# Kernel tuning notes

Measured on AMD Instinct MI355X. Metric: run time of the kernel, lower is better.

## Reference

```python
import jax, jax.numpy as jnp
import numpy as np

STRIDES = (8, 16, 32, 64)
IMG = 640
B, G, C = 32, 128, 80
REG_MAX = 7
CENTER_RADIUS = 2.5
TOPK = 10
IOU_W, CLS_W = 3.0, 1.0
VFL_ALPHA, VFL_GAMMA = 0.75, 2.0


def _make_priors():
    out = []
    for s in STRIDES:
        n = IMG // s
        ys = (np.arange(n, dtype=np.float32) + 0.5) * s
        xs = (np.arange(n, dtype=np.float32) + 0.5) * s
        yy, xx = np.meshgrid(ys, xs, indexing='ij')
        cx, cy = xx.ravel(), yy.ravel()
        ss = np.full_like(cx, float(s))
        out.append(np.stack([cx, cy, ss, ss], -1))
    return jnp.asarray(np.concatenate(out, 0), jnp.float32)  # (8500, 4)


def setup_inputs() -> dict:
    key = jax.random.key(0)
    k1, k2, k3, k4, k5, k6 = jax.random.split(key, 6)
    priors = _make_priors()
    N = priors.shape[0]
    # decoded xyxy boxes centered near each prior
    off = jax.random.normal(k1, (B, N, 2), dtype=jnp.float32) * 8.0
    wh = jax.random.uniform(k2, (B, N, 2), minval=8.0, maxval=160.0)
    ctr = priors[None, :, :2] + off
    decoded_bboxes = jnp.concatenate([ctr - wh * 0.5, ctr + wh * 0.5], -1)
    cls_pred = jax.random.uniform(k3, (B, N, C), minval=1e-4, maxval=1.0 - 1e-4)
    reg_pred = jax.random.normal(k4, (B, N, 4 * (REG_MAX + 1)), dtype=jnp.float32)
    gctr = jax.random.uniform(k5, (B, G, 2), minval=50.0, maxval=IMG - 50.0)
    gwh = jax.random.uniform(jax.random.fold_in(k5, 1), (B, G, 2), minval=20.0, maxval=300.0)
    gt_bboxes = jnp.concatenate([gctr - gwh * 0.5, gctr + gwh * 0.5], -1)
    gt_labels = jax.random.randint(k6, (B, G), 0, C)
    return {"priors": priors, "decoded_bboxes": decoded_bboxes, "cls_pred": cls_pred,
            "reg_pred": reg_pred, "gt_bboxes": gt_bboxes, "gt_labels": gt_labels}


def _pairwise_iou(a, b):
    # a: (N,4), b: (G,4) xyxy -> (N,G)
    area_a = (a[:, 2] - a[:, 0]) * (a[:, 3] - a[:, 1])
    area_b = (b[:, 2] - b[:, 0]) * (b[:, 3] - b[:, 1])
    tl = jnp.maximum(a[:, None, :2], b[None, :, :2])
    br = jnp.minimum(a[:, None, 2:], b[None, :, 2:])
    wh = jnp.clip(br - tl, 0.0)
    inter = wh[..., 0] * wh[..., 1]
    return inter / (area_a[:, None] + area_b[None, :] - inter + 1e-16)


def _giou_loss(pred, tgt):
    # aligned rows, xyxy; returns (N,)
    tl = jnp.maximum(pred[:, :2], tgt[:, :2])
    br = jnp.minimum(pred[:, 2:], tgt[:, 2:])
    wh = jnp.clip(br - tl, 0.0)
    inter = wh[:, 0] * wh[:, 1]
    ap = jnp.clip(pred[:, 2] - pred[:, 0], 0.0) * jnp.clip(pred[:, 3] - pred[:, 1], 0.0)
    at = jnp.clip(tgt[:, 2] - tgt[:, 0], 0.0) * jnp.clip(tgt[:, 3] - tgt[:, 1], 0.0)
    union = ap + at - inter
    iou = inter / (union + 1e-16)
    ctl = jnp.minimum(pred[:, :2], tgt[:, :2])
    cbr = jnp.maximum(pred[:, 2:], tgt[:, 2:])
    cwh = jnp.clip(cbr - ctl, 0.0)
    ac = cwh[:, 0] * cwh[:, 1]
    return 1.0 - (iou - (ac - union) / (ac + 1e-16))


def _simota(priors, dec, clsp, gtb, gtl):
    # single image. priors (N,4), dec (N,4), clsp (N,C), gtb (G,4), gtl (G,)
    nG = gtb.shape[0]
    cx, cy = priors[:, 0:1], priors[:, 1:2]
    sw, sh = priors[:, 2:3], priors[:, 3:4]
    # in-gt-box test: min of 4 edge distances > 0  -> (N,G)
    in_box = jnp.minimum(jnp.minimum(cx - gtb[None, :, 0], cy - gtb[None, :, 1]),
                         jnp.minimum(gtb[None, :, 2] - cx, gtb[None, :, 3] - cy)) > 0
    gcx = (gtb[:, 0] + gtb[:, 2]) * 0.5
    gcy = (gtb[:, 1] + gtb[:, 3]) * 0.5
    in_ctr = jnp.minimum(jnp.minimum(cx - (gcx[None] - CENTER_RADIUS * sw),
                                     cy - (gcy[None] - CENTER_RADIUS * sh)),
                         jnp.minimum(gcx[None] + CENTER_RADIUS * sw - cx,
                                     gcy[None] + CENTER_RADIUS * sh - cy)) > 0
    valid = in_box.any(1) | in_ctr.any(1)          # (N,)
    in_both = in_box & in_ctr                      # (N,G)
    ious = _pairwise_iou(dec, gtb)                 # (N,G)
    ious_m = jnp.where(valid[:, None], ious, 0.0)
    iou_cost = -jnp.log(ious + 1e-8)
    p = jnp.clip(clsp, 1e-7, 1.0 - 1e-7)
    neg = -jnp.log1p(-p)                           # (N,C)
    pos = -jnp.log(p)
    # sum_c BCE(p_nc, onehot_g) = sum_neg - neg[:,label_g] + pos[:,label_g]
    cls_cost = neg.sum(-1)[:, None] - neg[:, gtl] + pos[:, gtl]   # (N,G)
    cost = (CLS_W * cls_cost + IOU_W * iou_cost
            + 1e5 * (~in_both).astype(cost_dtype := clsp.dtype)
            + 1e8 * (~valid)[:, None].astype(cost_dtype))
    # dynamic-k per gt from sum of top-10 IoUs (invalid priors contribute 0)
    topk_ious = jax.lax.top_k(ious_m.T, TOPK)[0]                  # (G,TOPK)
    dyn_k = jnp.maximum(topk_ious.sum(-1).astype(jnp.int32), 1)   # (G,)
    # rank of each prior per gt (ascending cost); select dyn_k cheapest
    order = jnp.argsort(cost, axis=0)
    ranks = jnp.argsort(order, axis=0)
    matching = ranks < dyn_k[None, :]                             # (N,G) bool
    # resolve priors matched to >1 gt: keep lowest-cost gt
    multi = matching.sum(1) > 1
    best = jnp.argmin(cost, axis=1)
    matching = jnp.where(multi[:, None], jax.nn.one_hot(best, nG, dtype=bool), matching)
    fg = matching.any(1)
    mgt = jnp.argmax(matching, axis=1)
    mious = (matching * ious).sum(1)
    return fg, mgt, mious


def _image_loss(priors, dec, clsp, regp, gtb, gtl):
    sg = jax.lax.stop_gradient
    fg, mgt, mious = _simota(sg(priors), sg(dec), sg(clsp), sg(gtb), gtl)
    N = priors.shape[0]
    tscore = jnp.where(fg, mious, 0.0)             # (N,) soft target score
    lbl = gtl[mgt]                                 # (N,)
    # Varifocal loss (probabilities in, like the BCE-on-probs assigner)
    tgt = jax.nn.one_hot(lbl, C, dtype=clsp.dtype) * tscore[:, None]
    p = jnp.clip(clsp, 1e-7, 1.0 - 1e-7)
    bce = -(tgt * jnp.log(p) + (1.0 - tgt) * jnp.log1p(-p))
    w = jnp.where(tgt > 0, tgt, VFL_ALPHA * p ** VFL_GAMMA)
    vfl = (bce * w).sum()
    # GIoU on positives, weighted by target score
    ab = gtb[mgt]                                  # assigned gt box per prior (N,4)
    giou_sum = (_giou_loss(dec, ab) * tscore).sum()
    # DFL: distances from prior center to gt edges in stride units
    ctr, s = priors[:, :2], priors[:, 2:3]
    d = jnp.stack([ctr[:, 0] - ab[:, 0], ctr[:, 1] - ab[:, 1],
                   ab[:, 2] - ctr[:, 0], ab[:, 3] - ctr[:, 1]], -1) / s
    t = jnp.clip(d, 0.0, REG_MAX - 0.1)            # (N,4)
    logits = regp.reshape(N, 4, REG_MAX + 1)
    logp = jax.nn.log_softmax(logits, -1)
    tl_ = t.astype(jnp.int32)
    tr_ = jnp.minimum(tl_ + 1, REG_MAX)
    wl = (tl_ + 1).astype(t.dtype) - t
    wr = t - tl_.astype(t.dtype)
    ce = -(jnp.take_along_axis(logp, tl_[..., None], -1)[..., 0] * wl
           + jnp.take_along_axis(logp, tr_[..., None], -1)[..., 0] * wr)
    dfl_sum = (ce.sum(-1) * tscore).sum()
    return vfl, giou_sum, dfl_sum, fg.sum().astype(clsp.dtype), tscore.sum()


def _forward(priors, decoded_bboxes, cls_pred, reg_pred, gt_bboxes, gt_labels):
    vfl, gi, df, npos, nscore = jax.vmap(_image_loss, in_axes=(None, 0, 0, 0, 0, 0))(
        priors, decoded_bboxes, cls_pred, reg_pred, gt_bboxes, gt_labels)
    npos_t = jnp.maximum(npos.sum(), 1.0)
    ns_t = jnp.maximum(nscore.sum(), 1.0)
    return vfl.sum() / npos_t + 2.0 * gi.sum() / ns_t + 0.25 * df.sum() / ns_t


def reference(priors, decoded_bboxes, cls_pred, reg_pred, gt_bboxes, gt_labels):
    return _forward(priors, decoded_bboxes, cls_pred, reg_pred, gt_bboxes, gt_labels)
```

## Files before the change

kernel.cpp:

```cpp
#include <hip/hip_runtime.h>
#include <cstdint>
#include <cstddef>

#define NP    8500
#define BS    32
#define NGT   128
#define NCLS  80
#define TOPKK 10

typedef unsigned long long u64;
typedef unsigned int u32;

static __device__ __forceinline__ float iou_prec(const float4 a, const float4 b) {
  float area_a = (a.z - a.x) * (a.w - a.y);
  float area_b = (b.z - b.x) * (b.w - b.y);
  float tlx = fmaxf(a.x, b.x), tly = fmaxf(a.y, b.y);
  float brx = fminf(a.z, b.z), bry = fminf(a.w, b.w);
  float ww = fmaxf(brx - tlx, 0.f), hh = fmaxf(bry - tly, 0.f);
  float inter = ww * hh;
  return inter / (area_a + area_b - inter + 1e-16f);
}

static __device__ __forceinline__ float iou_fast(const float4 a, const float4 b) {
  float area_a = (a.z - a.x) * (a.w - a.y);
  float area_b = (b.z - b.x) * (b.w - b.y);
  float tlx = fmaxf(a.x, b.x), tly = fmaxf(a.y, b.y);
  float brx = fminf(a.z, b.z), bry = fminf(a.w, b.w);
  float ww = fmaxf(brx - tlx, 0.f), hh = fmaxf(bry - tly, 0.f);
  float inter = ww * hh;
  return __fdividef(inter, area_a + area_b - inter + 1e-16f);
}

static __device__ __forceinline__ float clampp(float p) {
  return fminf(fmaxf(p, 1e-7f), 1.0f - 1e-7f);
}

static __device__ __forceinline__ float wlog(float p) {
  return __logf((1.0f - p) / p);
}

static __device__ __forceinline__ u64 shflxor_u64(u64 v, int mask) {
  int lo = __shfl_xor((int)(u32)(v & 0xffffffffull), mask, 64);
  int hi = __shfl_xor((int)(u32)(v >> 32), mask, 64);
  return ((u64)(u32)hi << 32) | (u32)lo;
}

static __device__ __forceinline__ u32 f2u_mono(float f) {
  u32 b = __float_as_uint(f);
  return b ^ ((b & 0x80000000u) ? 0xffffffffu : 0x80000000u);
}

template<bool TR>
__global__ __launch_bounds__(256) void k_prep(
    const float* __restrict__ priors, const float* __restrict__ gtb,
    const float* __restrict__ clsp,
    float* __restrict__ negsum, unsigned char* __restrict__ valid,
    u64* __restrict__ inboth, float* __restrict__ ccostT)
{
  __shared__ float4 sg[NGT];
  const int b = blockIdx.y;
  const int tid = threadIdx.x;
  if (tid < NGT) sg[tid] = reinterpret_cast<const float4*>(gtb + (size_t)b * NGT * 4)[tid];
  __syncthreads();
  const int n = blockIdx.x * 256 + tid;
  if (n >= NP) return;
  const float4 pr = reinterpret_cast<const float4*>(priors)[n];
  const float cx = pr.x, cy = pr.y, sw = pr.z, sh = pr.w;
  u64 m0 = 0, m1 = 0;
  bool anyv = false;
  const float CR = 2.5f;
  for (int g = 0; g < NGT; ++g) {
    float4 gb = sg[g];
    float ib = fminf(fminf(cx - gb.x, cy - gb.y), fminf(gb.z - cx, gb.w - cy));
    bool in_box = ib > 0.f;
    float gcx = (gb.x + gb.z) * 0.5f, gcy = (gb.y + gb.w) * 0.5f;
    float ic = fminf(fminf(cx - (gcx - CR * sw), cy - (gcy - CR * sh)),
                     fminf(gcx + CR * sw - cx, gcy + CR * sh - cy));
    bool in_ctr = ic > 0.f;
    anyv |= (in_box | in_ctr);
    if (in_box && in_ctr) {
      if (g < 64) m0 |= 1ull << g; else m1 |= 1ull << (g - 64);
    }
  }
  const size_t idx = (size_t)b * NP + n;
  valid[idx] = anyv ? 1 : 0;
  inboth[idx * 2] = m0;
  inboth[idx * 2 + 1] = m1;

  const float4* row4 = reinterpret_cast<const float4*>(clsp + idx * NCLS);
  float s = 0.f;
  #pragma unroll 5
  for (int i = 0; i < NCLS / 4; ++i) {
    float4 p4 = row4[i];
    float q0 = 1.f - clampp(p4.x), q1 = 1.f - clampp(p4.y);
    float q2 = 1.f - clampp(p4.z), q3 = 1.f - clampp(p4.w);
    s -= __logf((q0 * q1) * (q2 * q3));
  }
  negsum[idx] = s;

  if (TR) {
    #pragma unroll 5
    for (int i = 0; i < NCLS / 4; ++i) {
      float4 p4 = row4[i];
      float w0 = wlog(clampp(p4.x)), w1 = wlog(clampp(p4.y));
      float w2 = wlog(clampp(p4.z)), w3 = wlog(clampp(p4.w));
      const size_t base = ((size_t)b * NCLS + i * 4) * NP + n;
      ccostT[base]          = s + w0;
      ccostT[base + NP]     = s + w1;
      ccostT[base + 2 * NP] = s + w2;
      ccostT[base + 3 * NP] = s + w3;
    }
  }
}

template<bool TR>
__global__ __launch_bounds__(64, 4) void k_assign(
    const float* __restrict__ dec, const float* __restrict__ gtb,
    const int* __restrict__ gtl, const float* __restrict__ clsp,
    const float* __restrict__ negsum, const unsigned char* __restrict__ valid,
    const u64* __restrict__ inboth, const float* __restrict__ ccostT,
    u64* __restrict__ match)
{
  const int wid = (int)((blockIdx.x & 7) * (gridDim.x >> 3) + (blockIdx.x >> 3));
  const int lane = threadIdx.x;
  const int b = wid >> 7;
  const int g = wid & 127;
  const float4 gb = reinterpret_cast<const float4*>(gtb)[b * NGT + g];
  const int l = gtl[b * NGT + g];
  const float4* decb = reinterpret_cast<const float4*>(dec) + (size_t)b * NP;
  const unsigned char* valb = valid + (size_t)b * NP;
  const u64* inbb = inboth + (size_t)b * NP * 2;
  const float* ccrow = TR ? (ccostT + ((size_t)b * NCLS + l) * NP) : nullptr;
  const float* negb = negsum + (size_t)b * NP;
  const float* clspb = clsp + (size_t)b * NP * NCLS;

  float t[TOPKK];
  u64 k[TOPKK];
  #pragma unroll
  for (int i = 0; i < TOPKK; ++i) { t[i] = 0.f; k[i] = ~0ull; }

  for (int n = lane; n < NP; n += 64) {
    const float4 db = decb[n];
    const bool vn = valb[n] != 0;
    const float iou = iou_fast(db, gb);
    const float v = vn ? iou : 0.f;
    if (v > t[0]) {
      t[0] = v;
      #pragma unroll
      for (int i = 0; i < TOPKK - 1; ++i) {
        if (t[i] > t[i + 1]) { float tmp = t[i]; t[i] = t[i + 1]; t[i + 1] = tmp; }
        else break;
      }
    }
    float base;
    if (TR) base = ccrow[n];
    else {
      float p = clampp(clspb[(size_t)n * NCLS + l]);
      base = negb[n] + wlog(p);
    }
    const bool inb = ((inbb[2 * (size_t)n + (g >> 6)] >> (g & 63)) & 1ull) != 0;
    float c = fmaf(-3.f, __logf(iou + 1e-8f), base);
    c += inb ? 0.f : 1e5f;
    c += vn ? 0.f : 1e8f;
    const u64 key = ((u64)f2u_mono(c) << 32) | (u32)n;
    if (key < k[TOPKK - 1]) {
      k[TOPKK - 1] = key;
      #pragma unroll
      for (int i = TOPKK - 1; i > 0; --i) {
        if (k[i] < k[i - 1]) { u64 tmp = k[i]; k[i] = k[i - 1]; k[i - 1] = tmp; }
        else break;
      }
    }
  }

  float sum = 0.f;
  #pragma unroll
  for (int r = 0; r < TOPKK; ++r) {
    float cand = t[TOPKK - 1];
    float m = cand;
    #pragma unroll
    for (int off = 32; off; off >>= 1) m = fmaxf(m, __shfl_xor(m, off, 64));
    sum += m;
    u64 ball = __ballot(cand == m);
    int win = __ffsll(ball) - 1;
    if (lane == win) {
      #pragma unroll
      for (int i = TOPKK - 1; i > 0; --i) t[i] = t[i - 1];
      t[0] = -1.f;
    }
  }
  int dynk = (int)sum;
  if (dynk < 1) dynk = 1;
  if (dynk > TOPKK) dynk = TOPKK;

  for (int r = 0; r < dynk; ++r) {
    u64 cand = k[0];
    u64 m = cand;
    #pragma unroll
    for (int off = 32; off; off >>= 1) {
      u64 o = shflxor_u64(m, off);
      if (o < m) m = o;
    }
    u64 ball = __ballot(cand == m);
    int win = __ffsll(ball) - 1;
    if (lane == win) {
      u32 nn = (u32)(m & 0xffffffffu);
      atomicOr(&match[((size_t)b * NP + nn) * 2 + (g >> 6)], 1ull << (g & 63));
      #pragma unroll
      for (int i = 0; i < TOPKK - 1; ++i) k[i] = k[i + 1];
      k[TOPKK - 1] = ~0ull;
    }
  }
}

template<bool TR>
__global__ __launch_bounds__(256) void k_post(
    const float* __restrict__ dec, const float* __restrict__ gtb,
    const int* __restrict__ gtl, const float* __restrict__ clsp,
    const float* __restrict__ negsum, const unsigned char* __restrict__ valid,
    const u64* __restrict__ inboth, const float* __restrict__ ccostT,
    const u64* __restrict__ match,
    float* __restrict__ tscore, int* __restrict__ mgt,
    float* __restrict__ p_np, float* __restrict__ p_ns)
{
  const int b = blockIdx.y;
  const int tid = threadIdx.x;
  const int n = blockIdx.x * 256 + tid;
  float ts = 0.f, fgf = 0.f;
  if (n < NP) {
    const size_t idx = (size_t)b * NP + n;
    u64 m0 = match[idx * 2], m1 = match[idx * 2 + 1];
    int pop = __popcll(m0) + __popcll(m1);
    int mg = 0;
    if (pop > 0) {
      fgf = 1.f;
      float4 db = reinterpret_cast<const float4*>(dec)[idx];
      int g;
      if (pop == 1) {
        g = m0 ? (__ffsll(m0) - 1) : (64 + __ffsll(m1) - 1);
      } else {
        bool vn = valid[idx] != 0;
        u64 ib0 = inboth[idx * 2], ib1 = inboth[idx * 2 + 1];
        float nsv = negsum[idx];
        float bc = 3.4e38f; int bg_ = 0;
        for (int gg = 0; gg < NGT; ++gg) {
          float4 gbv = reinterpret_cast<const float4*>(gtb)[b * NGT + gg];
          int lg_ = gtl[b * NGT + gg];
          float base;
          if (TR) base = ccostT[((size_t)b * NCLS + lg_) * NP + n];
          else    base = nsv + wlog(clampp(clsp[idx * NCLS + lg_]));
          bool inb = (((gg < 64) ? (ib0 >> gg) : (ib1 >> (gg - 64))) & 1ull) != 0;
          float iou = iou_fast(db, gbv);
          float c = fmaf(-3.f, __logf(iou + 1e-8f), base);
          c += inb ? 0.f : 1e5f;
          c += vn ? 0.f : 1e8f;
          if (c < bc) { bc = c; bg_ = gg; }
        }
        g = bg_;
      }
      mg = g;
      ts = iou_prec(db, reinterpret_cast<const float4*>(gtb)[b * NGT + g]);
    }
    tscore[idx] = ts;
    mgt[idx] = mg;
  }
  __shared__ float red[256];
  red[tid] = fgf; __syncthreads();
  for (int s = 128; s > 0; s >>= 1) { if (tid < s) red[tid] += red[tid + s]; __syncthreads(); }
  float npb = red[0]; __syncthreads();
  red[tid] = ts; __syncthreads();
  for (int s = 128; s > 0; s >>= 1) { if (tid < s) red[tid] += red[tid + s]; __syncthreads(); }
  if (tid == 0) {
    int blk = blockIdx.y * gridDim.x + blockIdx.x;
    p_np[blk] = npb;
    p_ns[blk] = red[0];
  }
}

__global__ __launch_bounds__(256) void k_loss(
    const float* __restrict__ priors, const float* __restrict__ dec,
    const float* __restrict__ clsp, const float* __restrict__ regp,
    const float* __restrict__ gtb, const int* __restrict__ gtl,
    const float* __restrict__ tscore, const int* __restrict__ mgt,
    float* __restrict__ p_vfl, float* __restrict__ p_gi, float* __restrict__ p_df)
{
  const int b = blockIdx.y;
  const int tid = threadIdx.x;
  const int n = blockIdx.x * 256 + tid;
  float vfl = 0.f, gi = 0.f, df = 0.f;
  if (n < NP) {
    const size_t idx = (size_t)b * NP + n;
    const float ts = tscore[idx];
    const int mg = mgt[idx];
    const float* row = clsp + idx * NCLS;
    const float4* row4 = reinterpret_cast<const float4*>(row);
    #pragma unroll 5
    for (int i = 0; i < NCLS / 4; ++i) {
      float4 p4 = row4[i];
      float ps[4] = {p4.x, p4.y, p4.z, p4.w};
      #pragma unroll
      for (int j = 0; j < 4; ++j) {
        float p = clampp(ps[j]);
        vfl += (-__logf(1.f - p)) * (0.75f * p * p);
      }
    }
    if (ts > 0.f) {
      const int lbl = gtl[b * NGT + mg];
      float p = clampp(row[lbl]);
      float l1 = __logf(1.f - p);
      vfl -= (-l1) * (0.75f * p * p);
      vfl += (-(ts * __logf(p) + (1.f - ts) * l1)) * ts;

      const float4 ab = reinterpret_cast<const float4*>(gtb)[b * NGT + mg];
      const float4 db = reinterpret_cast<const float4*>(dec)[idx];
      {
        float tlx = fmaxf(db.x, ab.x), tly = fmaxf(db.y, ab.y);
        float brx = fminf(db.z, ab.z), bry = fminf(db.w, ab.w);
        float iw = fmaxf(brx - tlx, 0.f), ih = fmaxf(bry - tly, 0.f);
        float inter = iw * ih;
        float ap = fmaxf(db.z - db.x, 0.f) * fmaxf(db.w - db.y, 0.f);
        float at = fmaxf(ab.z - ab.x, 0.f) * fmaxf(ab.w - ab.y, 0.f);
        float uni = ap + at - inter;
        float iou = inter / (uni + 1e-16f);
        float ctlx = fminf(db.x, ab.x), ctly = fminf(db.y, ab.y);
        float cbrx = fmaxf(db.z, ab.z), cbry = fmaxf(db.w, ab.w);
        float cw = fmaxf(cbrx - ctlx, 0.f), ch = fmaxf(cbry - ctly, 0.f);
        float ac = cw * ch;
        float gl = 1.f - (iou - (ac - uni) / (ac + 1e-16f));
        gi = gl * ts;
      }
      {
        const float4 pr = reinterpret_cast<const float4*>(priors)[n];
        const float s = pr.z;
        float dv[4] = {(pr.x - ab.x) / s, (pr.y - ab.y) / s,
                       (ab.z - pr.x) / s, (ab.w - pr.y) / s};
        const float* rrow = regp + idx * 32;
        float ce_sum = 0.f;
        #pragma unroll
        for (int side = 0; side < 4; ++side) {
          float tv = fminf(fmaxf(dv[side], 0.f), 6.9f);
          int tl_ = (int)tv;
          int tr_ = tl_ + 1; if (tr_ > 7) tr_ = 7;
          float wl = (float)(tl_ + 1) - tv;
          float wr = tv - (float)tl_;
          const float* lg = rrow + side * 8;
          float mx = lg[0];
          #pragma unroll
          for (int i = 1; i < 8; ++i) mx = fmaxf(mx, lg[i]);
          float se = 0.f;
          #pragma unroll
          for (int i = 0; i < 8; ++i) se += __expf(lg[i] - mx);
          float lse = __logf(se);
          float lp_tl = lg[tl_] - mx - lse;
          float lp_tr = lg[tr_] - mx - lse;
          ce_sum += -(lp_tl * wl + lp_tr * wr);
        }
        df = ce_sum * ts;
      }
    }
  }
  __shared__ float red[256];
  red[tid] = vfl; __syncthreads();
  for (int s = 128; s > 0; s >>= 1) { if (tid < s) red[tid] += red[tid + s]; __syncthreads(); }
  float vflb = red[0]; __syncthreads();
  red[tid] = gi; __syncthreads();
  for (int s = 128; s > 0; s >>= 1) { if (tid < s) red[tid] += red[tid + s]; __syncthreads(); }
  float gib = red[0]; __syncthreads();
  red[tid] = df; __syncthreads();
  for (int s = 128; s > 0; s >>= 1) { if (tid < s) red[tid] += red[tid + s]; __syncthreads(); }
  if (tid == 0) {
    int blk = blockIdx.y * gridDim.x + blockIdx.x;
    p_vfl[blk] = vflb;
    p_gi[blk] = gib;
    p_df[blk] = red[0];
  }
}

__global__ __launch_bounds__(256) void k_final(
    const float* __restrict__ p_vfl, const float* __restrict__ p_gi,
    const float* __restrict__ p_df, const float* __restrict__ p_np,
    const float* __restrict__ p_ns, float* __restrict__ out, int nb)
{
  __shared__ double red[256];
  const float* arrs[5] = {p_vfl, p_gi, p_df, p_np, p_ns};
  double sums[5];
  for (int a = 0; a < 5; ++a) {
    double s = 0.0;
    for (int i = threadIdx.x; i < nb; i += 256) s += (double)arrs[a][i];
    red[threadIdx.x] = s; __syncthreads();
    for (int st = 128; st > 0; st >>= 1) {
      if (threadIdx.x < st) red[threadIdx.x] += red[threadIdx.x + st];
      __syncthreads();
    }
    sums[a] = red[0]; __syncthreads();
  }
  if (threadIdx.x == 0) {
    double npos = sums[3] > 1.0 ? sums[3] : 1.0;
    double ns = sums[4] > 1.0 ? sums[4] : 1.0;
    out[0] = (float)(sums[0] / npos + 2.0 * sums[1] / ns + 0.25 * sums[2] / ns);
  }
}

extern "C" void kernel_launch(void* const* d_in, const int* in_sizes, int n_in,
                              void* d_out, int out_size, void* d_ws, size_t ws_size,
                              hipStream_t stream) {
  const float* priors = (const float*)d_in[0];
  const float* dec    = (const float*)d_in[1];
  const float* clsp   = (const float*)d_in[2];
  const float* regp   = (const float*)d_in[3];
  const float* gtb    = (const float*)d_in[4];
  const int*   gtl    = (const int*)d_in[5];
  float* out = (float*)d_out;

  char* w = (char*)d_ws;
  size_t off = 0;
  auto take = [&](size_t bytes) -> char* {
    char* p = w + off;
    off += (bytes + 255) & ~(size_t)255;
    return p;
  };
  float* negsum        = (float*)take((size_t)BS * NP * 4);
  unsigned char* valid = (unsigned char*)take((size_t)BS * NP);
  u64* inboth          = (u64*)take((size_t)BS * NP * 16);
  u64* match           = (u64*)take((size_t)BS * NP * 16);
  float* tscore        = (float*)take((size_t)BS * NP * 4);
  int* mgt             = (int*)take((size_t)BS * NP * 4);
  const int NBX = (NP + 255) / 256;
  const int NBLK = NBX * BS;
  float* p_vfl = (float*)take((size_t)NBLK * 4);
  float* p_gi  = (float*)take((size_t)NBLK * 4);
  float* p_df  = (float*)take((size_t)NBLK * 4);
  float* p_np  = (float*)take((size_t)NBLK * 4);
  float* p_ns  = (float*)take((size_t)NBLK * 4);
  const size_t ccost_bytes = (size_t)BS * NCLS * NP * 4;
  const bool useT = (off + ccost_bytes + 256) <= ws_size;
  float* ccostT = useT ? (float*)take(ccost_bytes) : nullptr;

  hipMemsetAsync(match, 0, (size_t)BS * NP * 16, stream);

  dim3 gridA(NBX, BS);
  if (useT) {
    k_prep<true><<<gridA, 256, 0, stream>>>(priors, gtb, clsp, negsum, valid, inboth, ccostT);
    k_assign<true><<<dim3(BS * NGT), 64, 0, stream>>>(dec, gtb, gtl, clsp, negsum,
                                                      valid, inboth, ccostT, match);
    k_post<true><<<gridA, 256, 0, stream>>>(dec, gtb, gtl, clsp, negsum, valid, inboth,
                                            ccostT, match, tscore, mgt, p_np, p_ns);
  } else {
    k_prep<false><<<gridA, 256, 0, stream>>>(priors, gtb, clsp, negsum, valid, inboth, nullptr);
    k_assign<false><<<dim3(BS * NGT), 64, 0, stream>>>(dec, gtb, gtl, clsp, negsum,
                                                       valid, inboth, nullptr, match);
    k_post<false><<<gridA, 256, 0, stream>>>(dec, gtb, gtl, clsp, negsum, valid, inboth,
                                             nullptr, match, tscore, mgt, p_np, p_ns);
  }
  k_loss<<<gridA, 256, 0, stream>>>(priors, dec, clsp, regp, gtb, gtl,
                                    tscore, mgt, p_vfl, p_gi, p_df);
  k_final<<<1, 256, 0, stream>>>(p_vfl, p_gi, p_df, p_np, p_ns, out, NBLK);
}
```

Before: 504.4 us.

## Use wave-cooperative threshold candidate buffering for top-k and fuse post with loss

The per-lane sorted top-k insertion in k_assign is replaced with a wave-wide threshold filter. Candidates beating the current 10th-best are compacted into shared memory via ballot, then merged with shuffle reductions when the buffer fills, which cuts per-element divergent sorting and the register pressure of holding per-lane top-10 arrays. k_post and k_loss are fused into one kernel that caches GT boxes and labels in shared memory and no longer writes tscore/mgt to memory. The ccostT path is now mandatory, dropping the workspace-size fallback, which risks failure if the workspace is too small.

```diff
diff --git a/kernel.cpp b/kernel.cpp
--- a/kernel.cpp
+++ b/kernel.cpp
@@ -50,7 +50,6 @@
   return b ^ ((b & 0x80000000u) ? 0xffffffffu : 0x80000000u);
 }
 
-template<bool TR>
 __global__ __launch_bounds__(256) void k_prep(
     const float* __restrict__ priors, const float* __restrict__ gtb,
     const float* __restrict__ clsp,
@@ -98,29 +97,33 @@
   }
   negsum[idx] = s;
 
-  if (TR) {
-    #pragma unroll 5
-    for (int i = 0; i < NCLS / 4; ++i) {
-      float4 p4 = row4[i];
-      float w0 = wlog(clampp(p4.x)), w1 = wlog(clampp(p4.y));
-      float w2 = wlog(clampp(p4.z)), w3 = wlog(clampp(p4.w));
-      const size_t base = ((size_t)b * NCLS + i * 4) * NP + n;
-      ccostT[base]          = s + w0;
-      ccostT[base + NP]     = s + w1;
-      ccostT[base + 2 * NP] = s + w2;
-      ccostT[base + 3 * NP] = s + w3;
-    }
-  }
-}
-
-template<bool TR>
+  #pragma unroll 5
+  for (int i = 0; i < NCLS / 4; ++i) {
+    float4 p4 = row4[i];
+    float w0 = wlog(clampp(p4.x)), w1 = wlog(clampp(p4.y));
+    float w2 = wlog(clampp(p4.z)), w3 = wlog(clampp(p4.w));
+    const size_t base = ((size_t)b * NCLS + i * 4) * NP + n;
+    ccostT[base]          = s + w0;
+    ccostT[base + NP]     = s + w1;
+    ccostT[base + 2 * NP] = s + w2;
+    ccostT[base + 3 * NP] = s + w3;
+  }
+}
+
+#define CAND_CAP 128
+#define CAND_TRIG 48
 __global__ __launch_bounds__(64, 4) void k_assign(
     const float* __restrict__ dec, const float* __restrict__ gtb,
-    const int* __restrict__ gtl, const float* __restrict__ clsp,
-    const float* __restrict__ negsum, const unsigned char* __restrict__ valid,
+    const int* __restrict__ gtl,
+    const unsigned char* __restrict__ valid,
     const u64* __restrict__ inboth, const float* __restrict__ ccostT,
     u64* __restrict__ match)
 {
+  __shared__ float ibuf[CAND_CAP];
+  __shared__ u64  kbuf[CAND_CAP];
+  __shared__ float cur_i[TOPKK];
+  __shared__ u64  cur_k[TOPKK];
+
   const int wid = (int)((blockIdx.x & 7) * (gridDim.x >> 3) + (blockIdx.x >> 3));
   const int lane = threadIdx.x;
   const int b = wid >> 7;
@@ -129,170 +132,160 @@
   const int l = gtl[b * NGT + g];
   const float4* decb = reinterpret_cast<const float4*>(dec) + (size_t)b * NP;
   const unsigned char* valb = valid + (size_t)b * NP;
-  const u64* inbb = inboth + (size_t)b * NP * 2;
-  const float* ccrow = TR ? (ccostT + ((size_t)b * NCLS + l) * NP) : nullptr;
-  const float* negb = negsum + (size_t)b * NP;
-  const float* clspb = clsp + (size_t)b * NP * NCLS;
-
-  float t[TOPKK];
-  u64 k[TOPKK];
-  #pragma unroll
-  for (int i = 0; i < TOPKK; ++i) { t[i] = 0.f; k[i] = ~0ull; }
-
-  for (int n = lane; n < NP; n += 64) {
+  const u64* inbb = inboth + (size_t)b * NP * 2 + (g >> 6);
+  const float* ccrow = ccostT + ((size_t)b * NCLS + l) * NP;
+  const u64 gbit = 1ull << (g & 63);
+  const u64 lanemask_lt = (1ull << lane) - 1ull;
+
+  float taui = -1.f;
+  u64  tauk = ~0ull;
+  int icnt = 0, kcnt = 0;
+  bool merged_i = false, merged_k = false;
+
+  auto merge_i = [&]() {
+    if (merged_i && lane == 0) {
+      #pragma unroll
+      for (int r = 0; r < TOPKK; ++r) ibuf[icnt + r] = cur_i[r];
+    }
+    int total = icnt + (merged_i ? TOPKK : 0);
+    __threadfence_block();
+    float c0 = (lane < total) ? ibuf[lane] : -3.4e38f;
+    float c1 = (64 + lane < total) ? ibuf[64 + lane] : -3.4e38f;
+    #pragma unroll
+    for (int r = 0; r < TOPKK; ++r) {
+      float cm = fmaxf(c0, c1);
+      float mr = cm;
+      #pragma unroll
+      for (int off = 32; off; off >>= 1) mr = fmaxf(mr, __shfl_xor(mr, off, 64));
+      u64 bal = __ballot(cm == mr);
+      int win = __ffsll(bal) - 1;
+      if (lane == win) { if (c0 == mr) c0 = -3.4e38f; else c1 = -3.4e38f; }
+      if (lane == 0) cur_i[r] = mr;
+      taui = mr;
+    }
+    icnt = 0; merged_i = true;
+  };
+  auto merge_k = [&]() {
+    if (merged_k && lane == 0) {
+      #pragma unroll
+      for (int r = 0; r < TOPKK; ++r) kbuf[kcnt + r] = cur_k[r];
+    }
+    int total = kcnt + (merged_k ? TOPKK : 0);
+    __threadfence_block();
+    u64 c0 = (lane < total) ? kbuf[lane] : ~0ull;
+    u64 c1 = (64 + lane < total) ? kbuf[64 + lane] : ~0ull;
+    #pragma unroll
+    for (int r = 0; r < TOPKK; ++r) {
+      u64 cm = (c0 < c1) ? c0 : c1;
+      u64 mr = cm;
+      #pragma unroll
+      for (int off = 32; off; off >>= 1) {
+        u64 o = shflxor_u64(mr, off);
+        if (o < mr) mr = o;
+      }
+      u64 bal = __ballot(cm == mr);
+      int win = __ffsll(bal) - 1;
+      if (lane == win) { if (c0 == mr) c0 = ~0ull; else c1 = ~0ull; }
+      if (lane == 0) cur_k[r] = mr;
+      tauk = mr;
+    }
+    kcnt = 0; merged_k = true;
+  };
+
+  for (int base = 0; base < NP; base += 64) {
+    const int n0 = base + lane;
+    const int n = (n0 < NP) ? n0 : (NP - 1);
+    const bool inrange = (n0 < NP);
     const float4 db = decb[n];
     const bool vn = valb[n] != 0;
     const float iou = iou_fast(db, gb);
     const float v = vn ? iou : 0.f;
-    if (v > t[0]) {
-      t[0] = v;
-      #pragma unroll
-      for (int i = 0; i < TOPKK - 1; ++i) {
-        if (t[i] > t[i + 1]) { float tmp = t[i]; t[i] = t[i + 1]; t[i + 1] = tmp; }
-        else break;
-      }
-    }
-    float base;
-    if (TR) base = ccrow[n];
-    else {
-      float p = clampp(clspb[(size_t)n * NCLS + l]);
-      base = negb[n] + wlog(p);
-    }
-    const bool inb = ((inbb[2 * (size_t)n + (g >> 6)] >> (g & 63)) & 1ull) != 0;
-    float c = fmaf(-3.f, __logf(iou + 1e-8f), base);
+
+    bool ci = inrange & (v > taui);
+    u64 bal = __ballot(ci);
+    if (ci) ibuf[icnt + __popcll(bal & lanemask_lt)] = v;
+    icnt += (int)__popcll(bal);
+
+    float c = fmaf(-3.f, __logf(iou + 1e-8f), ccrow[n]);
+    const bool inb = ((inbb[2 * (size_t)n] & gbit) != 0);
     c += inb ? 0.f : 1e5f;
     c += vn ? 0.f : 1e8f;
     const u64 key = ((u64)f2u_mono(c) << 32) | (u32)n;
-    if (key < k[TOPKK - 1]) {
-      k[TOPKK - 1] = key;
-      #pragma unroll
-      for (int i = TOPKK - 1; i > 0; --i) {
-        if (k[i] < k[i - 1]) { u64 tmp = k[i]; k[i] = k[i - 1]; k[i - 1] = tmp; }
-        else break;
-      }
-    }
-  }
+    bool ck = inrange & (key < tauk);
+    bal = __ballot(ck);
+    if (ck) kbuf[kcnt + __popcll(bal & lanemask_lt)] = key;
+    kcnt += (int)__popcll(bal);
+
+    if (icnt > CAND_TRIG) merge_i();
+    if (kcnt > CAND_TRIG) merge_k();
+  }
+  if (icnt > 0) merge_i();
+  if (kcnt > 0) merge_k();
+  __threadfence_block();
 
   float sum = 0.f;
   #pragma unroll
-  for (int r = 0; r < TOPKK; ++r) {
-    float cand = t[TOPKK - 1];
-    float m = cand;
-    #pragma unroll
-    for (int off = 32; off; off >>= 1) m = fmaxf(m, __shfl_xor(m, off, 64));
-    sum += m;
-    u64 ball = __ballot(cand == m);
-    int win = __ffsll(ball) - 1;
-    if (lane == win) {
-      #pragma unroll
-      for (int i = TOPKK - 1; i > 0; --i) t[i] = t[i - 1];
-      t[0] = -1.f;
-    }
-  }
+  for (int r = 0; r < TOPKK; ++r) sum += cur_i[r];
   int dynk = (int)sum;
   if (dynk < 1) dynk = 1;
   if (dynk > TOPKK) dynk = TOPKK;
 
-  for (int r = 0; r < dynk; ++r) {
-    u64 cand = k[0];
-    u64 m = cand;
-    #pragma unroll
-    for (int off = 32; off; off >>= 1) {
-      u64 o = shflxor_u64(m, off);
-      if (o < m) m = o;
-    }
-    u64 ball = __ballot(cand == m);
-    int win = __ffsll(ball) - 1;
-    if (lane == win) {
-      u32 nn = (u32)(m & 0xffffffffu);
-      atomicOr(&match[((size_t)b * NP + nn) * 2 + (g >> 6)], 1ull << (g & 63));
-      #pragma unroll
-      for (int i = 0; i < TOPKK - 1; ++i) k[i] = k[i + 1];
-      k[TOPKK - 1] = ~0ull;
-    }
-  }
-}
-
-template<bool TR>
-__global__ __launch_bounds__(256) void k_post(
-    const float* __restrict__ dec, const float* __restrict__ gtb,
-    const int* __restrict__ gtl, const float* __restrict__ clsp,
+  if (lane < dynk) {
+    u32 nn = (u32)(cur_k[lane] & 0xffffffffu);
+    atomicOr(&match[((size_t)b * NP + nn) * 2 + (g >> 6)], gbit);
+  }
+}
+
+__global__ __launch_bounds__(256) void k_postloss(
+    const float* __restrict__ priors, const float* __restrict__ dec,
+    const float* __restrict__ clsp, const float* __restrict__ regp,
+    const float* __restrict__ gtb, const int* __restrict__ gtl,
     const float* __restrict__ negsum, const unsigned char* __restrict__ valid,
-    const u64* __restrict__ inboth, const float* __restrict__ ccostT,
-    const u64* __restrict__ match,
-    float* __restrict__ tscore, int* __restrict__ mgt,
+    const u64* __restrict__ inboth, const u64* __restrict__ match,
+    float* __restrict__ p_vfl, float* __restrict__ p_gi, float* __restrict__ p_df,
     float* __restrict__ p_np, float* __restrict__ p_ns)
 {
+  __shared__ float4 sg[NGT];
+  __shared__ int sl[NGT];
   const int b = blockIdx.y;
   const int tid = threadIdx.x;
+  if (tid < NGT) {
+    sg[tid] = reinterpret_cast<const float4*>(gtb + (size_t)b * NGT * 4)[tid];
+    sl[tid] = gtl[b * NGT + tid];
+  }
+  __syncthreads();
   const int n = blockIdx.x * 256 + tid;
-  float ts = 0.f, fgf = 0.f;
+  float ts = 0.f, fgf = 0.f, vfl = 0.f, gi = 0.f, df = 0.f;
   if (n < NP) {
     const size_t idx = (size_t)b * NP + n;
+    const float* row = clsp + idx * NCLS;
     u64 m0 = match[idx * 2], m1 = match[idx * 2 + 1];
     int pop = __popcll(m0) + __popcll(m1);
     int mg = 0;
+    float4 db;
     if (pop > 0) {
       fgf = 1.f;
-      float4 db = reinterpret_cast<const float4*>(dec)[idx];
-      int g;
+      db = reinterpret_cast<const float4*>(dec)[idx];
       if (pop == 1) {
-        g = m0 ? (__ffsll(m0) - 1) : (64 + __ffsll(m1) - 1);
+        mg = m0 ? (__ffsll(m0) - 1) : (64 + __ffsll(m1) - 1);
       } else {
         bool vn = valid[idx] != 0;
         u64 ib0 = inboth[idx * 2], ib1 = inboth[idx * 2 + 1];
         float nsv = negsum[idx];
-        float bc = 3.4e38f; int bg_ = 0;
+        float bc = 3.4e38f;
         for (int gg = 0; gg < NGT; ++gg) {
-          float4 gbv = reinterpret_cast<const float4*>(gtb)[b * NGT + gg];
-          int lg_ = gtl[b * NGT + gg];
-          float base;
-          if (TR) base = ccostT[((size_t)b * NCLS + lg_) * NP + n];
-          else    base = nsv + wlog(clampp(clsp[idx * NCLS + lg_]));
+          float base = nsv + wlog(clampp(row[sl[gg]]));
           bool inb = (((gg < 64) ? (ib0 >> gg) : (ib1 >> (gg - 64))) & 1ull) != 0;
-          float iou = iou_fast(db, gbv);
+          float iou = iou_fast(db, sg[gg]);
           float c = fmaf(-3.f, __logf(iou + 1e-8f), base);
           c += inb ? 0.f : 1e5f;
           c += vn ? 0.f : 1e8f;
-          if (c < bc) { bc = c; bg_ = gg; }
+          if (c < bc) { bc = c; mg = gg; }
         }
-        g = bg_;
       }
-      mg = g;
-      ts = iou_prec(db, reinterpret_cast<const float4*>(gtb)[b * NGT + g]);
-    }
-    tscore[idx] = ts;
-    mgt[idx] = mg;
-  }
-  __shared__ float red[256];
-  red[tid] = fgf; __syncthreads();
-  for (int s = 128; s > 0; s >>= 1) { if (tid < s) red[tid] += red[tid + s]; __syncthreads(); }
-  float npb = red[0]; __syncthreads();
-  red[tid] = ts; __syncthreads();
-  for (int s = 128; s > 0; s >>= 1) { if (tid < s) red[tid] += red[tid + s]; __syncthreads(); }
-  if (tid == 0) {
-    int blk = blockIdx.y * gridDim.x + blockIdx.x;
-    p_np[blk] = npb;
-    p_ns[blk] = red[0];
-  }
-}
-
-__global__ __launch_bounds__(256) void k_loss(
-    const float* __restrict__ priors, const float* __restrict__ dec,
-    const float* __restrict__ clsp, const float* __restrict__ regp,
-    const float* __restrict__ gtb, const int* __restrict__ gtl,
-    const float* __restrict__ tscore, const int* __restrict__ mgt,
-    float* __restrict__ p_vfl, float* __restrict__ p_gi, float* __restrict__ p_df)
-{
-  const int b = blockIdx.y;
-  const int tid = threadIdx.x;
-  const int n = blockIdx.x * 256 + tid;
-  float vfl = 0.f, gi = 0.f, df = 0.f;
-  if (n < NP) {
-    const size_t idx = (size_t)b * NP + n;
-    const float ts = tscore[idx];
-    const int mg = mgt[idx];
-    const float* row = clsp + idx * NCLS;
+      ts = iou_prec(db, sg[mg]);
+    }
+
     const float4* row4 = reinterpret_cast<const float4*>(row);
     #pragma unroll 5
     for (int i = 0; i < NCLS / 4; ++i) {
@@ -305,14 +298,13 @@
       }
     }
     if (ts > 0.f) {
-      const int lbl = gtl[b * NGT + mg];
+      const int lbl = sl[mg];
       float p = clampp(row[lbl]);
       float l1 = __logf(1.f - p);
       vfl -= (-l1) * (0.75f * p * p);
       vfl += (-(ts * __logf(p) + (1.f - ts) * l1)) * ts;
 
-      const float4 ab = reinterpret_cast<const float4*>(gtb)[b * NGT + mg];
-      const float4 db = reinterpret_cast<const float4*>(dec)[idx];
+      const float4 ab = sg[mg];
       {
         float tlx = fmaxf(db.x, ab.x), tly = fmaxf(db.y, ab.y);
         float brx = fminf(db.z, ab.z), bry = fminf(db.w, ab.w);
@@ -360,19 +352,22 @@
     }
   }
   __shared__ float red[256];
-  red[tid] = vfl; __syncthreads();
-  for (int s = 128; s > 0; s >>= 1) { if (tid < s) red[tid] += red[tid + s]; __syncthreads(); }
-  float vflb = red[0]; __syncthreads();
-  red[tid] = gi; __syncthreads();
-  for (int s = 128; s > 0; s >>= 1) { if (tid < s) red[tid] += red[tid + s]; __syncthreads(); }
-  float gib = red[0]; __syncthreads();
-  red[tid] = df; __syncthreads();
-  for (int s = 128; s > 0; s >>= 1) { if (tid < s) red[tid] += red[tid + s]; __syncthreads(); }
+  float acc[5] = {vfl, gi, df, fgf, ts};
+  float out5[5];
+  #pragma unroll
+  for (int a = 0; a < 5; ++a) {
+    __syncthreads();
+    red[tid] = acc[a]; __syncthreads();
+    for (int s = 128; s > 0; s >>= 1) { if (tid < s) red[tid] += red[tid + s]; __syncthreads(); }
+    out5[a] = red[0];
+  }
   if (tid == 0) {
     int blk = blockIdx.y * gridDim.x + blockIdx.x;
-    p_vfl[blk] = vflb;
-    p_gi[blk] = gib;
-    p_df[blk] = red[0];
+    p_vfl[blk] = out5[0];
+    p_gi[blk]  = out5[1];
+    p_df[blk]  = out5[2];
+    p_np[blk]  = out5[3];
+    p_ns[blk]  = out5[4];
   }
 }
 
@@ -423,8 +418,6 @@
   unsigned char* valid = (unsigned char*)take((size_t)BS * NP);
   u64* inboth          = (u64*)take((size_t)BS * NP * 16);
   u64* match           = (u64*)take((size_t)BS * NP * 16);
-  float* tscore        = (float*)take((size_t)BS * NP * 4);
-  int* mgt             = (int*)take((size_t)BS * NP * 4);
   const int NBX = (NP + 255) / 256;
   const int NBLK = NBX * BS;
   float* p_vfl = (float*)take((size_t)NBLK * 4);
@@ -432,27 +425,15 @@
   float* p_df  = (float*)take((size_t)NBLK * 4);
   float* p_np  = (float*)take((size_t)NBLK * 4);
   float* p_ns  = (float*)take((size_t)NBLK * 4);
-  const size_t ccost_bytes = (size_t)BS * NCLS * NP * 4;
-  const bool useT = (off + ccost_bytes + 256) <= ws_size;
-  float* ccostT = useT ? (float*)take(ccost_bytes) : nullptr;
+  float* ccostT = (float*)take((size_t)BS * NCLS * NP * 4);
 
   hipMemsetAsync(match, 0, (size_t)BS * NP * 16, stream);
 
   dim3 gridA(NBX, BS);
-  if (useT) {
-    k_prep<true><<<gridA, 256, 0, stream>>>(priors, gtb, clsp, negsum, valid, inboth, ccostT);
-    k_assign<true><<<dim3(BS * NGT), 64, 0, stream>>>(dec, gtb, gtl, clsp, negsum,
-                                                      valid, inboth, ccostT, match);
-    k_post<true><<<gridA, 256, 0, stream>>>(dec, gtb, gtl, clsp, negsum, valid, inboth,
-                                            ccostT, match, tscore, mgt, p_np, p_ns);
-  } else {
-    k_prep<false><<<gridA, 256, 0, stream>>>(priors, gtb, clsp, negsum, valid, inboth, nullptr);
-    k_assign<false><<<dim3(BS * NGT), 64, 0, stream>>>(dec, gtb, gtl, clsp, negsum,
-                                                       valid, inboth, nullptr, match);
-    k_post<false><<<gridA, 256, 0, stream>>>(dec, gtb, gtl, clsp, negsum, valid, inboth,
-                                             nullptr, match, tscore, mgt, p_np, p_ns);
-  }
-  k_loss<<<gridA, 256, 0, stream>>>(priors, dec, clsp, regp, gtb, gtl,
-                                    tscore, mgt, p_vfl, p_gi, p_df);
+  k_prep<<<gridA, 256, 0, stream>>>(priors, gtb, clsp, negsum, valid, inboth, ccostT);
+  k_assign<<<dim3(BS * NGT), 64, 0, stream>>>(dec, gtb, gtl, valid, inboth, ccostT, match);
+  k_postloss<<<gridA, 256, 0, stream>>>(priors, dec, clsp, regp, gtb, gtl,
+                                        negsum, valid, inboth, match,
+                                        p_vfl, p_gi, p_df, p_np, p_ns);
   k_final<<<1, 256, 0, stream>>>(p_vfl, p_gi, p_df, p_np, p_ns, out, NBLK);
 }
```

After: 523.5 us. +3.8%, slower.
